# Optimization experiments

Measured on AMD Instinct MI355X. Metric: run time of the kernel, lower is better.

## Reference

```python
import jax, jax.numpy as jnp
import numpy as np

LN_EPS = 1e-12
NEG_INF = -1e9


def setup_inputs() -> dict:
    key = jax.random.key(0)
    ks = jax.random.split(key, 4)
    B, S, H = 8, 2048, 1024
    inputs = jax.random.normal(ks[0], (B, S, H), dtype=jnp.float32)
    masks = jnp.ones((B, S), dtype=jnp.int32)
    scale = 1.0 / np.sqrt(H)
    Wq = jax.random.normal(ks[1], (H, H), dtype=jnp.float32) * scale
    bq = jnp.zeros((H,), dtype=jnp.float32)
    Wk = jax.random.normal(ks[2], (H, H), dtype=jnp.float32) * scale
    bk = jnp.zeros((H,), dtype=jnp.float32)
    ln_gamma = jnp.ones((H,), dtype=jnp.float32)
    ln_beta = jnp.zeros((H,), dtype=jnp.float32)
    return {"inputs": inputs, "masks": masks, "Wq": Wq, "bq": bq,
            "Wk": Wk, "bk": bk, "ln_gamma": ln_gamma, "ln_beta": ln_beta}


def _layernorm(x, gamma, beta):
    mu = jnp.mean(x, axis=-1, keepdims=True)
    var = jnp.mean(jnp.square(x - mu), axis=-1, keepdims=True)
    return (x - mu) * jax.lax.rsqrt(var + LN_EPS) * gamma + beta


def reference(inputs, masks, Wq, bq, Wk, bk, ln_gamma, ln_beta):
    # inputs: [B,S,H]; masks: [B,S] (1 = keep key position)
    H = inputs.shape[-1]
    query = inputs @ Wq + bq                      # [B,S,H]
    key_ = inputs @ Wk + bk                       # [B,S,H]
    scores = jnp.einsum('bqh,bkh->bqk', query, key_) * (1.0 / jnp.sqrt(jnp.float32(H)))
    # logits_mask: invalid key positions get large negative logit
    scores = jnp.where(masks[:, None, :] != 0, scores, NEG_INF)
    probs = jax.nn.softmax(scores, axis=-1)       # [B,S,S]
    context = jnp.einsum('bqk,bkh->bqh', probs, inputs)  # value = raw inputs
    return _layernorm(inputs + context, ln_gamma, ln_beta)
```

## Files before the change

### kernel.cpp

```cpp
#include <hip/hip_runtime.h>
#include <stdint.h>
#include <stddef.h>

typedef _Float16 f16_t;
typedef _Float16 f16x8 __attribute__((ext_vector_type(8)));
typedef _Float16 f16x4 __attribute__((ext_vector_type(4)));
typedef float    f32x4 __attribute__((ext_vector_type(4)));

#define AS_G __attribute__((address_space(1)))
#define AS_L __attribute__((address_space(3)))

__device__ __forceinline__ void gload_lds16(const void* g, void* l) {
  __builtin_amdgcn_global_load_lds((const AS_G uint32_t*)g, (AS_L uint32_t*)l, 16, 0, 0);
}

__device__ __forceinline__ void stage8(const f16_t* g, int ld, char* l) {
#pragma unroll
  for (int j = 0; j < 4; ++j)
    gload_lds16(g + (size_t)(j * 8) * ld, l + j * 1024);
}

#define LN_EPS 1e-12f

__global__ __launch_bounds__(256) void cast_f16_kernel(const float* __restrict__ in,
                                                       f16_t* __restrict__ out) {
  int i = blockIdx.x * 256 + threadIdx.x;
  float4 v = ((const float4*)in)[i];
  f16x4 o = {(f16_t)v.x, (f16_t)v.y, (f16_t)v.z, (f16_t)v.w};
  ((f16x4*)out)[i] = o;
}

__global__ __launch_bounds__(256) void xprep_kernel(const float* __restrict__ in,
                                                    f16_t* __restrict__ xb,
                                                    f16_t* __restrict__ xt) {
  __shared__ float tile[32][33];
  int b = blockIdx.z;
  const float* inb = in + (size_t)b * 2048 * 1024;
  f16_t* xbb = xb + (size_t)b * 2048 * 1024;
  f16_t* xtb = xt + (size_t)b * 1024 * 2048;
  int tx = threadIdx.x, ty = threadIdx.y;
  int c0 = blockIdx.x * 32, r0 = blockIdx.y * 32;
#pragma unroll
  for (int i = 0; i < 32; i += 8) {
    float v = inb[(size_t)(r0 + ty + i) * 1024 + (c0 + tx)];
    tile[ty + i][tx] = v;
    xbb[(size_t)(r0 + ty + i) * 1024 + (c0 + tx)] = (f16_t)v;
  }
  __syncthreads();
#pragma unroll
  for (int i = 0; i < 32; i += 8)
    xtb[(size_t)(c0 + ty + i) * 2048 + (r0 + tx)] = (f16_t)tile[tx][ty + i];
}

__global__ __launch_bounds__(256) void wvec_kernel(const float* __restrict__ Wq,
                                                   const float* __restrict__ bq,
                                                   const float* __restrict__ Wk,
                                                   const float* __restrict__ bk,
                                                   float* __restrict__ wqbk,
                                                   float* __restrict__ wkbq,
                                                   float* __restrict__ c0) {
  __shared__ float red[4];
  int bid = blockIdx.x, tid = threadIdx.x;
  const float* rowp; const float* vecp; float* outp;
  if (bid < 1024)      { rowp = Wq + (size_t)bid * 1024; vecp = bk; outp = wqbk + bid; }
  else if (bid < 2048) { rowp = Wk + (size_t)(bid - 1024) * 1024; vecp = bq; outp = wkbq + (bid - 1024); }
  else                 { rowp = bq; vecp = bk; outp = c0; }
  float4 a = ((const float4*)rowp)[tid];
  float4 b = ((const float4*)vecp)[tid];
  float s = a.x * b.x + a.y * b.y + a.z * b.z + a.w * b.w;
#pragma unroll
  for (int off = 32; off > 0; off >>= 1) s += __shfl_xor(s, off, 64);
  if ((tid & 63) == 0) red[tid >> 6] = s;
  __syncthreads();
  if (tid == 0) *outp = red[0] + red[1] + red[2] + red[3];
}

__global__ __launch_bounds__(256) void cqck_kernel(const float* __restrict__ X,
                                                   const float* __restrict__ wqbk,
                                                   const float* __restrict__ wkbq,
                                                   float* __restrict__ cq,
                                                   float* __restrict__ ck) {
  __shared__ float r1[4], r2[4];
  int m = blockIdx.x, tid = threadIdx.x;
  float4 x = ((const float4*)(X + (size_t)m * 1024))[tid];
  float4 a = ((const float4*)wqbk)[tid];
  float4 b = ((const float4*)wkbq)[tid];
  float s1 = x.x * a.x + x.y * a.y + x.z * a.z + x.w * a.w;
  float s2 = x.x * b.x + x.y * b.y + x.z * b.z + x.w * b.w;
#pragma unroll
  for (int off = 32; off > 0; off >>= 1) { s1 += __shfl_xor(s1, off, 64); s2 += __shfl_xor(s2, off, 64); }
  if ((tid & 63) == 0) { r1[tid >> 6] = s1; r2[tid >> 6] = s2; }
  __syncthreads();
  if (tid == 0) {
    cq[m] = r1[0] + r1[1] + r1[2] + r1[3];
    ck[m] = r2[0] + r2[1] + r2[2] + r2[3];
  }
}

__global__ __launch_bounds__(256) void gemm_bt_kernel(
    const f16_t* __restrict__ A, const f16_t* __restrict__ Bt, f16_t* __restrict__ C,
    int lda, int ldb, int ldc, int K) {
  __shared__ f16_t As[2][128 * 64];
  __shared__ f16_t Bs[2][128 * 64];

  const int tid = threadIdx.x;
  const int lane = tid & 63;
  const int wv = tid >> 6;
  const int m16 = lane & 15;
  const int quad = lane >> 4;
  const int wr = (wv >> 1) * 64;
  const int wc = (wv & 1) * 64;

  const f16_t* Ab = A + (size_t)blockIdx.x * 128 * lda;
  const f16_t* Bb = Bt + (size_t)blockIdx.y * 128 * ldb;

  const int lr8 = lane >> 3;
  const int ch8 = (lane & 7) ^ lr8;
  const f16_t* gA[4]; const f16_t* gB[4];
  f16_t* lA[4]; f16_t* lB[4];
#pragma unroll
  for (int j = 0; j < 4; ++j) {
    int row = wv * 32 + j * 8 + lr8;
    gA[j] = Ab + (size_t)row * lda + ch8 * 8;
    gB[j] = Bb + (size_t)row * ldb + ch8 * 8;
    lA[j] = &As[0][(wv * 32 + j * 8) * 64];
    lB[j] = &Bs[0][(wv * 32 + j * 8) * 64];
  }

  int aoff[4], boff[4], swz[2];
#pragma unroll
  for (int t = 0; t < 4; ++t) {
    aoff[t] = (wr + t * 16 + m16) * 64;
    boff[t] = (wc + t * 16 + m16) * 64;
  }
#pragma unroll
  for (int s = 0; s < 2; ++s)
    swz[s] = (((s << 2) | quad) ^ (m16 & 7)) * 8;

  f32x4 acc[4][4] = {};

#define STAGE(BUF, KOFF)                                       \
  _Pragma("unroll")                                            \
  for (int j = 0; j < 4; ++j) {                                \
    gload_lds16(gA[j] + (KOFF), lA[j] + (BUF) * (128 * 64));   \
    gload_lds16(gB[j] + (KOFF), lB[j] + (BUF) * (128 * 64));   \
  }

#define COMPUTE(BUF)                                                           \
  _Pragma("unroll")                                                            \
  for (int s = 0; s < 2; ++s) {                                                \
    f16x8 af[4], bfr[4];                                                       \
    _Pragma("unroll")                                                          \
    for (int t = 0; t < 4; ++t) {                                              \
      af[t]  = *(const f16x8*)&As[BUF][aoff[t] + swz[s]];                      \
      bfr[t] = *(const f16x8*)&Bs[BUF][boff[t] + swz[s]];                      \
    }                                                                          \
    _Pragma("unroll")                                                          \
    for (int rt = 0; rt < 4; ++rt)                                             \
      _Pragma("unroll")                                                        \
      for (int ct = 0; ct < 4; ++ct)                                           \
        acc[rt][ct] = __builtin_amdgcn_mfma_f32_16x16x32_f16(af[rt], bfr[ct],  \
                                                             acc[rt][ct], 0, 0, 0); \
  }

  STAGE(0, 0);
  __syncthreads();
  for (int k0 = 0; k0 < K; k0 += 128) {
    STAGE(1, k0 + 64);
    COMPUTE(0);
    __syncthreads();
    if (k0 + 128 < K) STAGE(0, k0 + 128);
    COMPUTE(1);
    __syncthreads();
  }
#undef STAGE
#undef COMPUTE

  const int row0 = blockIdx.x * 128 + wr + quad * 4;
  const int col0 = blockIdx.y * 128 + wc + m16;
#pragma unroll
  for (int ct = 0; ct < 4; ++ct)
#pragma unroll
    for (int rt = 0; rt < 4; ++rt)
#pragma unroll
      for (int r = 0; r < 4; ++r)
        C[(size_t)(row0 + rt * 16 + r) * ldc + col0 + ct * 16] = (f16_t)acc[rt][ct][r];
}

__global__ __launch_bounds__(512) void gemm256_kernel(
    const f16_t* __restrict__ A, const f16_t* __restrict__ Bt, f16_t* __restrict__ C,
    const float* __restrict__ cq, const float* __restrict__ ck, const float* __restrict__ c0p,
    const int* __restrict__ mask, const float* __restrict__ invl, float* __restrict__ lpart,
    int lda, int ldb, int ldc, int K, float scale, int mode,
    size_t sA, size_t sB, size_t sC) {
  __shared__ f16_t As[256 * 64];
  __shared__ f16_t Bs[256 * 64];

  const int tid = threadIdx.x;
  const int lane = tid & 63;
  const int wid = tid >> 6;
  const int wm = wid >> 2;
  const int wn = wid & 3;
  const int m16 = lane & 15;
  const int quad = lane >> 4;

  const f16_t* Ab = A + blockIdx.z * sA + (size_t)blockIdx.x * 256 * lda;
  const f16_t* Bb = Bt + blockIdx.z * sB + (size_t)blockIdx.y * 256 * ldb;

  const int lr8 = lane >> 3;
  const int ch8 = (lane & 7) ^ lr8;
  const f16_t* gA = Ab + (size_t)(wid * 32 + lr8) * lda + ch8 * 8;
  const f16_t* gB = Bb + (size_t)(wid * 32 + lr8) * ldb + ch8 * 8;
  char* ldsA = (char*)As + wid * 4096;
  char* ldsB = (char*)Bs + wid * 4096;

  int aoff[8], boff[4], swz[2];
#pragma unroll
  for (int mr = 0; mr < 8; ++mr) aoff[mr] = (wm * 128 + mr * 16 + m16) * 64;
#pragma unroll
  for (int nr = 0; nr < 4; ++nr) boff[nr] = (wn * 64 + nr * 16 + m16) * 64;
#pragma unroll
  for (int s = 0; s < 2; ++s)
    swz[s] = (((s << 2) | quad) ^ (m16 & 7)) * 8;

  f32x4 acc[8][4] = {};

  for (int k0 = 0; k0 < K; k0 += 64) {
    stage8(gA + k0, lda, ldsA);
    stage8(gB + k0, ldb, ldsB);
    __syncthreads();
#pragma unroll
    for (int s = 0; s < 2; ++s) {
      f16x8 af[8], bf[4];
#pragma unroll
      for (int mr = 0; mr < 8; ++mr) af[mr] = *(const f16x8*)&As[aoff[mr] + swz[s]];
#pragma unroll
      for (int nr = 0; nr < 4; ++nr) bf[nr] = *(const f16x8*)&Bs[boff[nr] + swz[s]];
#pragma unroll
      for (int mr = 0; mr < 8; ++mr)
#pragma unroll
        for (int nr = 0; nr < 4; ++nr)
          acc[mr][nr] = __builtin_amdgcn_mfma_f32_16x16x32_f16(af[mr], bf[nr],
                                                               acc[mr][nr], 0, 0, 0);
    }
    __syncthreads();
  }

  f16_t* Cb = C + blockIdx.z * sC;
  const int row0 = blockIdx.x * 256 + wm * 128 + quad * 4;
  const int col0 = blockIdx.y * 256 + wn * 64 + m16;
  if (mode == 0) {
#pragma unroll
    for (int nr = 0; nr < 4; ++nr)
#pragma unroll
      for (int mr = 0; mr < 8; ++mr)
#pragma unroll
        for (int r = 0; r < 4; ++r)
          Cb[(size_t)(row0 + mr * 16 + r) * ldc + col0 + nr * 16] = (f16_t)acc[mr][nr][r];
  } else if (mode == 1) {
    const int* mp = mask + blockIdx.z * 2048;
    const size_t rowg0 = blockIdx.z * 2048 + row0;
    const float c0 = *c0p;
    float rsum[8][4];
#pragma unroll
    for (int mr = 0; mr < 8; ++mr)
#pragma unroll
      for (int r = 0; r < 4; ++r) rsum[mr][r] = 0.f;
#pragma unroll
    for (int nr = 0; nr < 4; ++nr) {
      int col = col0 + nr * 16;
      bool keep = (mp[col] != 0);
      float ckv = ck[blockIdx.z * 2048 + col];
#pragma unroll
      for (int mr = 0; mr < 8; ++mr)
#pragma unroll
        for (int r = 0; r < 4; ++r) {
          float cqv = cq[rowg0 + mr * 16 + r];
          float p = keep ? __expf((acc[mr][nr][r] + cqv + ckv + c0) * scale) : 0.f;
          rsum[mr][r] += p;
          Cb[(size_t)(row0 + mr * 16 + r) * ldc + col] = (f16_t)p;
        }
    }
    const int chunk = blockIdx.y * 4 + wn;
#pragma unroll
    for (int mr = 0; mr < 8; ++mr)
#pragma unroll
      for (int r = 0; r < 4; ++r) {
        float v = rsum[mr][r];
        v += __shfl_xor(v, 1, 16);
        v += __shfl_xor(v, 2, 16);
        v += __shfl_xor(v, 4, 16);
        v += __shfl_xor(v, 8, 16);
        if (m16 == 0) lpart[(rowg0 + mr * 16 + r) * 32 + chunk] = v;
      }
  } else {
    const size_t rowg0 = blockIdx.z * 2048 + row0;
#pragma unroll
    for (int mr = 0; mr < 8; ++mr)
#pragma unroll
      for (int r = 0; r < 4; ++r) {
        float il = invl[rowg0 + mr * 16 + r];
#pragma unroll
        for (int nr = 0; nr < 4; ++nr)
          Cb[(size_t)(row0 + mr * 16 + r) * ldc + col0 + nr * 16] = (f16_t)(acc[mr][nr][r] * il);
      }
  }
}

__global__ __launch_bounds__(256) void lreduce_kernel(const float* __restrict__ lpart,
                                                      float* __restrict__ invl) {
  int m = blockIdx.x * 256 + threadIdx.x;
  const float4* p = (const float4*)(lpart + (size_t)m * 32);
  float s = 0.f;
#pragma unroll
  for (int j = 0; j < 8; ++j) {
    float4 v = p[j];
    s += v.x + v.y + v.z + v.w;
  }
  invl[m] = 1.0f / fmaxf(s, 1e-30f);
}

__global__ __launch_bounds__(256) void ln_kernel(const float* __restrict__ X,
                                                 const f16_t* __restrict__ Ctx,
                                                 const float* __restrict__ gamma,
                                                 const float* __restrict__ beta,
                                                 float* __restrict__ out) {
  __shared__ float r1[4], r2[4];
  const int tid = threadIdx.x;
  const size_t base = (size_t)blockIdx.x * 1024;
  float4 xv = ((const float4*)(X + base))[tid];
  f16x4 cv = ((const f16x4*)(Ctx + base))[tid];
  float v0 = xv.x + (float)cv[0];
  float v1 = xv.y + (float)cv[1];
  float v2 = xv.z + (float)cv[2];
  float v3 = xv.w + (float)cv[3];
  float s1 = v0 + v1 + v2 + v3;
  float s2 = v0 * v0 + v1 * v1 + v2 * v2 + v3 * v3;
#pragma unroll
  for (int off = 32; off > 0; off >>= 1) {
    s1 += __shfl_xor(s1, off, 64);
    s2 += __shfl_xor(s2, off, 64);
  }
  if ((tid & 63) == 0) { r1[tid >> 6] = s1; r2[tid >> 6] = s2; }
  __syncthreads();
  s1 = r1[0] + r1[1] + r1[2] + r1[3];
  s2 = r2[0] + r2[1] + r2[2] + r2[3];
  float mu = s1 * (1.0f / 1024.0f);
  float var = s2 * (1.0f / 1024.0f) - mu * mu;
  float rs = rsqrtf(fmaxf(var, 0.0f) + LN_EPS);
  float4 gv = ((const float4*)gamma)[tid];
  float4 bv = ((const float4*)beta)[tid];
  float4 o;
  o.x = (v0 - mu) * rs * gv.x + bv.x;
  o.y = (v1 - mu) * rs * gv.y + bv.y;
  o.z = (v2 - mu) * rs * gv.z + bv.z;
  o.w = (v3 - mu) * rs * gv.w + bv.w;
  ((float4*)(out + base))[tid] = o;
}

extern "C" void kernel_launch(void* const* d_in, const int* in_sizes, int n_in,
                              void* d_out, int out_size, void* d_ws, size_t ws_size,
                              hipStream_t stream) {
  const float* X     = (const float*)d_in[0];
  const int*   masks = (const int*)d_in[1];
  const float* Wq    = (const float*)d_in[2];
  const float* bq    = (const float*)d_in[3];
  const float* Wk    = (const float*)d_in[4];
  const float* bk    = (const float*)d_in[5];
  const float* gamma = (const float*)d_in[6];
  const float* beta  = (const float*)d_in[7];
  float* out = (float*)d_out;

  if (ws_size < 115343360u) return;
  char* ws = (char*)d_ws;
  f16_t* Xb   = (f16_t*)(ws + 0);
  f16_t* Xt   = (f16_t*)(ws + 33554432);
  f16_t* T    = (f16_t*)(ws + 67108864);
  f16_t* Wqf  = (f16_t*)(ws + 100663296);
  f16_t* Wkf  = (f16_t*)(ws + 102760448);
  f16_t* Wkq  = (f16_t*)(ws + 104857600);
  float* lpart= (float*)(ws + 106954752);
  float* cq   = (float*)(ws + 109051904);
  float* ck   = (float*)(ws + 109117440);
  float* invl = (float*)(ws + 109182976);
  float* wqbk = (float*)(ws + 109248512);
  float* wkbq = (float*)(ws + 109252608);
  float* c0   = (float*)(ws + 109256704);
  f16_t* Ctx  = Xb;
  f16_t* probs = (f16_t*)d_out;

  const size_t SH = 2048u * 1024u;
  const size_t SS = 2048u * 2048u;
  const size_t HS = 1024u * 2048u;

  xprep_kernel<<<dim3(32, 64, 8), dim3(32, 8), 0, stream>>>(X, Xb, Xt);
  cast_f16_kernel<<<1024, 256, 0, stream>>>(Wq, Wqf);
  cast_f16_kernel<<<1024, 256, 0, stream>>>(Wk, Wkf);
  wvec_kernel<<<2049, 256, 0, stream>>>(Wq, bq, Wk, bk, wqbk, wkbq, c0);
  cqck_kernel<<<16384, 256, 0, stream>>>(X, wqbk, wkbq, cq, ck);

  gemm_bt_kernel<<<dim3(8, 8, 1), 256, 0, stream>>>(
      Wkf, Wqf, Wkq, 1024, 1024, 1024, 1024);

  gemm256_kernel<<<dim3(64, 4, 1), 512, 0, stream>>>(
      Xb, Wkq, T, nullptr, nullptr, nullptr, nullptr, nullptr, nullptr,
      1024, 1024, 1024, 1024, 0.f, 0, 0, 0, 0);

  gemm256_kernel<<<dim3(8, 8, 8), 512, 0, stream>>>(
      T, Xb, probs, cq, ck, c0, masks, nullptr, lpart,
      1024, 1024, 2048, 1024, 0.03125f, 1, SH, SH, SS);

  lreduce_kernel<<<64, 256, 0, stream>>>(lpart, invl);

  gemm256_kernel<<<dim3(8, 4, 8), 512, 0, stream>>>(
      probs, Xt, Ctx, nullptr, nullptr, nullptr, nullptr, invl, nullptr,
      2048, 2048, 1024, 2048, 0.f, 2, SS, HS, SH);

  ln_kernel<<<16384, 256, 0, stream>>>(X, Ctx, gamma, beta, out);
}
```

Before: 490.9 us.

## Double-buffer LDS in gemm256 to overlap global loads with MFMA

```diff
diff --git a/kernel.cpp b/kernel.cpp
--- a/kernel.cpp
+++ b/kernel.cpp
@@ -193,8 +193,8 @@
     const int* __restrict__ mask, const float* __restrict__ invl, float* __restrict__ lpart,
     int lda, int ldb, int ldc, int K, float scale, int mode,
     size_t sA, size_t sB, size_t sC) {
-  __shared__ f16_t As[256 * 64];
-  __shared__ f16_t Bs[256 * 64];
+  __shared__ f16_t As[2][256 * 64];
+  __shared__ f16_t Bs[2][256 * 64];
 
   const int tid = threadIdx.x;
   const int lane = tid & 63;
@@ -225,62 +225,79 @@
 
   f32x4 acc[8][4] = {};
 
-  for (int k0 = 0; k0 < K; k0 += 64) {
-    stage8(gA + k0, lda, ldsA);
-    stage8(gB + k0, ldb, ldsB);
+#define STAGE(BUF, KOFF)                                 \
+  stage8(gA + (KOFF), lda, ldsA + (BUF) * 32768);        \
+  stage8(gB + (KOFF), ldb, ldsB + (BUF) * 32768);
+
+#define COMPUTE(BUF)                                                           \
+  _Pragma("unroll")                                                            \
+  for (int s = 0; s < 2; ++s) {                                                \
+    f16x8 af[8], bf[4];                                                        \
+    _Pragma("unroll")                                                          \
+    for (int mr = 0; mr < 8; ++mr) af[mr] = *(const f16x8*)&As[BUF][aoff[mr] + swz[s]]; \
+    _Pragma("unroll")                                                          \
+    for (int nr = 0; nr < 4; ++nr) bf[nr] = *(const f16x8*)&Bs[BUF][boff[nr] + swz[s]]; \
+    _Pragma("unroll")                                                          \
+    for (int mr = 0; mr < 8; ++mr)                                             \
+      _Pragma("unroll")                                                        \
+      for (int nr = 0; nr < 4; ++nr)                                           \
+        acc[mr][nr] = __builtin_amdgcn_mfma_f32_16x16x32_f16(af[mr], bf[nr],   \
+                                                             acc[mr][nr], 0, 0, 0); \
+  }
+
+  STAGE(0, 0);
+  __syncthreads();
+  for (int k0 = 0; k0 < K; k0 += 128) {
+    STAGE(1, k0 + 64);
+    COMPUTE(0);
     __syncthreads();
-#pragma unroll
-    for (int s = 0; s < 2; ++s) {
-      f16x8 af[8], bf[4];
-#pragma unroll
-      for (int mr = 0; mr < 8; ++mr) af[mr] = *(const f16x8*)&As[aoff[mr] + swz[s]];
-#pragma unroll
-      for (int nr = 0; nr < 4; ++nr) bf[nr] = *(const f16x8*)&Bs[boff[nr] + swz[s]];
-#pragma unroll
-      for (int mr = 0; mr < 8; ++mr)
-#pragma unroll
-        for (int nr = 0; nr < 4; ++nr)
-          acc[mr][nr] = __builtin_amdgcn_mfma_f32_16x16x32_f16(af[mr], bf[nr],
-                                                               acc[mr][nr], 0, 0, 0);
-    }
+    if (k0 + 128 < K) STAGE(0, k0 + 128);
+    COMPUTE(1);
     __syncthreads();
   }
+#undef STAGE
+#undef COMPUTE
 
   f16_t* Cb = C + blockIdx.z * sC;
   const int row0 = blockIdx.x * 256 + wm * 128 + quad * 4;
   const int col0 = blockIdx.y * 256 + wn * 64 + m16;
   if (mode == 0) {
 #pragma unroll
-    for (int nr = 0; nr < 4; ++nr)
-#pragma unroll
-      for (int mr = 0; mr < 8; ++mr)
-#pragma unroll
-        for (int r = 0; r < 4; ++r)
-          Cb[(size_t)(row0 + mr * 16 + r) * ldc + col0 + nr * 16] = (f16_t)acc[mr][nr][r];
+    for (int mr = 0; mr < 8; ++mr)
+#pragma unroll
+      for (int r = 0; r < 4; ++r) {
+        f16_t* rowp = Cb + (size_t)(row0 + mr * 16 + r) * ldc + col0;
+#pragma unroll
+        for (int nr = 0; nr < 4; ++nr)
+          rowp[nr * 16] = (f16_t)acc[mr][nr][r];
+      }
   } else if (mode == 1) {
     const int* mp = mask + blockIdx.z * 2048;
     const size_t rowg0 = blockIdx.z * 2048 + row0;
     const float c0 = *c0p;
-    float rsum[8][4];
-#pragma unroll
-    for (int mr = 0; mr < 8; ++mr)
-#pragma unroll
-      for (int r = 0; r < 4; ++r) rsum[mr][r] = 0.f;
+    float ckv[4]; bool keep[4];
 #pragma unroll
     for (int nr = 0; nr < 4; ++nr) {
       int col = col0 + nr * 16;
-      bool keep = (mp[col] != 0);
-      float ckv = ck[blockIdx.z * 2048 + col];
-#pragma unroll
-      for (int mr = 0; mr < 8; ++mr)
-#pragma unroll
-        for (int r = 0; r < 4; ++r) {
-          float cqv = cq[rowg0 + mr * 16 + r];
-          float p = keep ? __expf((acc[mr][nr][r] + cqv + ckv + c0) * scale) : 0.f;
-          rsum[mr][r] += p;
-          Cb[(size_t)(row0 + mr * 16 + r) * ldc + col] = (f16_t)p;
+      keep[nr] = (mp[col] != 0);
+      ckv[nr] = ck[blockIdx.z * 2048 + col];
+    }
+    float rsum[8][4];
+#pragma unroll
+    for (int mr = 0; mr < 8; ++mr)
+#pragma unroll
+      for (int r = 0; r < 4; ++r) {
+        float cqv = cq[rowg0 + mr * 16 + r];
+        f16_t* rowp = Cb + (size_t)(row0 + mr * 16 + r) * ldc + col0;
+        float rs_ = 0.f;
+#pragma unroll
+        for (int nr = 0; nr < 4; ++nr) {
+          float p = keep[nr] ? __expf((acc[mr][nr][r] + cqv + ckv[nr] + c0) * scale) : 0.f;
+          rs_ += p;
+          rowp[nr * 16] = (f16_t)p;
         }
-    }
+        rsum[mr][r] = rs_;
+      }
     const int chunk = blockIdx.y * 4 + wn;
 #pragma unroll
     for (int mr = 0; mr < 8; ++mr)
@@ -300,9 +317,10 @@
 #pragma unroll
       for (int r = 0; r < 4; ++r) {
         float il = invl[rowg0 + mr * 16 + r];
+        f16_t* rowp = Cb + (size_t)(row0 + mr * 16 + r) * ldc + col0;
 #pragma unroll
         for (int nr = 0; nr < 4; ++nr)
-          Cb[(size_t)(row0 + mr * 16 + r) * ldc + col0 + nr * 16] = (f16_t)(acc[mr][nr][r] * il);
+          rowp[nr * 16] = (f16_t)(acc[mr][nr][r] * il);
       }
   }
 }
```

After: 425.0 us. 1.15x faster.
